# Performance work log

Hardware: AMD Instinct MI355X
Metric: run time of the kernel (lower is better)

## Reference

```python
import jax, jax.numpy as jnp
import numpy as np

B, IN_DIM, HID, OUT_DIM = 32768, 784, 256, 1000
L, CURV = 3, 1e-3
LOG2_H = 8  # log2(HID)
EPS_BN = 1e-5

def _layer_param_sizes():
    return [(HID // (2 * (1 << (l % LOG2_H)))) * 2 for l in range(L)]

def setup_inputs():
    key = jax.random.key(0)
    ks = jax.random.split(key, 4)
    total = sum(_layer_param_sizes())  # 448
    return {
        "x": jax.random.normal(ks[0], (B, IN_DIM), jnp.float32),
        "fc1_w": jax.random.normal(ks[1], (HID, IN_DIM), jnp.float32) / np.sqrt(IN_DIM).astype(np.float32),
        "fc1_b": jnp.zeros((HID,), jnp.float32),
        "bn1_gamma": jnp.ones((HID,), jnp.float32),
        "bn1_beta": jnp.zeros((HID,), jnp.float32),
        "bf_params": jax.random.normal(ks[2], (total,), jnp.float32) * 0.01,
        "bn2_gamma": jnp.ones((HID,), jnp.float32),
        "bn2_beta": jnp.zeros((HID,), jnp.float32),
        "fc2_w": jax.random.normal(ks[3], (OUT_DIM, HID), jnp.float32) / np.sqrt(HID).astype(np.float32),
        "fc2_b": jnp.zeros((OUT_DIM,), jnp.float32),
    }

def _batchnorm(h, gamma, beta):
    # training-mode BatchNorm1d: batch mean / biased variance
    mu = jnp.mean(h, axis=0)
    var = jnp.mean(jnp.square(h - mu), axis=0)
    return gamma * (h - mu) * jax.lax.rsqrt(var + EPS_BN) + beta

def _log_map0(x, c):
    # Poincare ball log map at origin: artanh(sqrt(c)|x|) * x / (sqrt(c)|x|)
    sn = jnp.sqrt(c) * jnp.linalg.norm(x, axis=-1, keepdims=True)
    sn = jnp.clip(sn, 1e-7, 1.0 - 1e-6)
    return (jnp.arctanh(sn) / sn) * x

def _exp_map0(u, c):
    sn = jnp.maximum(jnp.sqrt(c) * jnp.linalg.norm(u, axis=-1, keepdims=True), 1e-7)
    return (jnp.tanh(sn) / sn) * u

def _hyper_butterfly(h, params, c):
    u = _log_map0(h, c)
    off = 0
    for l in range(L):
        bs = 1 << (l % LOG2_H)      # half-block size at stage l
        nb = HID // (2 * bs)        # number of 2x2-rotation blocks
        p = params[off:off + 2 * nb]
        a = p[:nb][None, :, None]   # [1, nb, 1]
        b = p[nb:][None, :, None]
        v = u.reshape(-1, nb, 2, bs)
        x1, x2 = v[:, :, 0], v[:, :, 1]
        y1 = a * x1 + b * x2
        y2 = -b * x1 + a * x2
        u = jnp.stack([y1, y2], axis=2).reshape(-1, HID)
        off += 2 * nb
    return _exp_map0(u, c)

def reference(x, fc1_w, fc1_b, bn1_gamma, bn1_beta, bf_params, bn2_gamma, bn2_beta, fc2_w, fc2_b):
    h = x @ fc1_w.T + fc1_b
    h = jax.nn.relu(_batchnorm(h, bn1_gamma, bn1_beta))
    ht = _hyper_butterfly(h, bf_params, CURV)
    ht = jax.nn.relu(_batchnorm(ht, bn2_gamma, bn2_beta))
    return ht @ fc2_w.T + fc2_b
```

## Files before the change

### kernel.cpp

```cpp
#include <hip/hip_runtime.h>
#include <math.h>

#define NBATCH 32768
#define IND    784
#define KPAD1  832
#define HIDD   256
#define OUTD   1000
#define OUTDP  1024

typedef _Float16 half8  __attribute__((ext_vector_type(8)));
typedef _Float16 half4v __attribute__((ext_vector_type(4)));
typedef float    floatx4 __attribute__((ext_vector_type(4)));

#define GAS __attribute__((address_space(1)))
#define LAS __attribute__((address_space(3)))

#define WAITVM(N) asm volatile("s_waitcnt vmcnt(" #N ")" ::: "memory")
#define WAITVM_BAR(N)                                                      \
    asm volatile("s_waitcnt vmcnt(" #N ") lgkmcnt(0)" ::: "memory");       \
    __builtin_amdgcn_s_barrier();                                          \
    __builtin_amdgcn_sched_barrier(0)

__device__ __forceinline__ void gld16(const void* g, void* l) {
    __builtin_amdgcn_global_load_lds((const GAS void*)g, (LAS void*)l, 16, 0, 0);
}

__device__ __forceinline__ float wave_allreduce_sum(float v) {
    #pragma unroll
    for (int off = 32; off >= 1; off >>= 1) v += __shfl_xor(v, off);
    return v;
}

__device__ __forceinline__ float fast_atanh(float s) {
    return 0.5f * __logf((1.0f + s) * __frcp_rn(1.0f - s));
}
__device__ __forceinline__ float fast_tanh(float x) {
    const float e = __expf(-2.0f * x);
    return (1.0f - e) * __frcp_rn(1.0f + e);
}

__global__ __launch_bounds__(256)
void prep_kernel(const float* __restrict__ w1, _Float16* __restrict__ w1h,
                 const float* __restrict__ w2, _Float16* __restrict__ w2h,
                 float* __restrict__ stat)
{
    const int tid = threadIdx.x;
    if (blockIdx.x == 0) {
        for (int j = tid; j < 1024 + 16; j += 256) stat[j] = 0.0f;
    }
    const int NW1 = HIDD * (KPAD1 / 8);
    const int NW2 = OUTDP * (HIDD / 8);
    for (int i = blockIdx.x * 256 + tid; i < NW1 + NW2; i += (int)gridDim.x * 256) {
        half8 o;
        if (i < NW1) {
            const int r = i / (KPAD1 / 8), c8 = (i % (KPAD1 / 8)) * 8;
            if (c8 + 8 <= IND) {
                const float* s = &w1[(size_t)r * IND + c8];
                float4 v0 = *(const float4*)s, v1 = *(const float4*)(s + 4);
                o[0]=(_Float16)v0.x; o[1]=(_Float16)v0.y; o[2]=(_Float16)v0.z; o[3]=(_Float16)v0.w;
                o[4]=(_Float16)v1.x; o[5]=(_Float16)v1.y; o[6]=(_Float16)v1.z; o[7]=(_Float16)v1.w;
            } else {
                #pragma unroll
                for (int j = 0; j < 8; ++j) o[j] = (_Float16)0.0f;
            }
            *(half8*)&w1h[(size_t)r * KPAD1 + c8] = o;
        } else {
            const int k = i - NW1;
            const int r = k >> 5, c8 = (k & 31) * 8;
            if (r < OUTD) {
                const float* s = &w2[(size_t)r * HIDD + c8];
                float4 v0 = *(const float4*)s, v1 = *(const float4*)(s + 4);
                o[0]=(_Float16)v0.x; o[1]=(_Float16)v0.y; o[2]=(_Float16)v0.z; o[3]=(_Float16)v0.w;
                o[4]=(_Float16)v1.x; o[5]=(_Float16)v1.y; o[6]=(_Float16)v1.z; o[7]=(_Float16)v1.w;
            } else {
                #pragma unroll
                for (int j = 0; j < 8; ++j) o[j] = (_Float16)0.0f;
            }
            *(half8*)&w2h[(size_t)r * HIDD + c8] = o;
        }
    }
}

__global__ __launch_bounds__(256, 2)
void gemm1_kernel(const float* __restrict__ x, const _Float16* __restrict__ w1h,
                  const float* __restrict__ b1, const float* __restrict__ zbuf,
                  _Float16* __restrict__ h16, float* __restrict__ sum1, float* __restrict__ ssq1)
{
    __shared__ __align__(16) _Float16 ldsA[2][8192];
    __shared__ __align__(16) _Float16 ldsB[2][8192];
    __shared__ float redS[2][128], redQ[2][128];

    const int tid  = threadIdx.x;
    const int bid0 = blockIdx.x;
    const int vbid = (bid0 & 7) * 64 + (bid0 >> 3);
    const int bm = vbid >> 1, bn = vbid & 1;
    const int m0 = bm * 128, n0 = bn * 128;
    const int lane = tid & 63, wv = tid >> 6;
    const int wr = wv >> 1, wc = wv & 1;
    const int l15 = lane & 15, lg = lane >> 4;
    const int e3 = l15 & 3;
    const int nt = KPAD1 / 64;

    const int r0g = tid >> 2, r1g = 64 + (tid >> 2), kq = tid & 3;
    const int wpos0 = r0g * 32 + ((kq ^ (r0g & 3)) * 8);
    const int wpos1 = r1g * 32 + ((kq ^ (r1g & 3)) * 8);
    const float* Ab0 = x + (size_t)(m0 + r0g) * IND + kq * 8;
    const float* Ab1 = x + (size_t)(m0 + r1g) * IND + kq * 8;

    const int brow = lane >> 2, bgp = (lane & 3) ^ (brow & 3);
    const _Float16* Bb = w1h + (size_t)(n0 + brow) * KPAD1 + bgp * 8;

    floatx4 acc[4][4];
    #pragma unroll
    for (int i = 0; i < 4; ++i)
        #pragma unroll
        for (int j = 0; j < 4; ++j) acc[i][j] = (floatx4){0.f, 0.f, 0.f, 0.f};

    floatx4 rgaE[8], rgaO[8];

    auto A_ISSUE = [&](floatx4 (&rg)[8], int t) {
        #pragma unroll
        for (int ks = 0; ks < 2; ++ks) {
            const int off = t * 64 + ks * 32;
            const bool v = (off + kq * 8) < IND;
            const float* p0 = v ? (Ab0 + off) : zbuf;
            const float* p1 = v ? (Ab1 + off) : zbuf;
            rg[ks*4+0] = *(const floatx4*)p0;
            rg[ks*4+1] = *(const floatx4*)(p0 + 4);
            rg[ks*4+2] = *(const floatx4*)p1;
            rg[ks*4+3] = *(const floatx4*)(p1 + 4);
        }
    };
    auto A_WRITE = [&](floatx4 (&rg)[8], int wb) {
        #pragma unroll
        for (int ks = 0; ks < 2; ++ks) {
            half8 h0, h1;
            #pragma unroll
            for (int j = 0; j < 4; ++j) {
                h0[j] = (_Float16)rg[ks*4+0][j]; h0[4+j] = (_Float16)rg[ks*4+1][j];
                h1[j] = (_Float16)rg[ks*4+2][j]; h1[4+j] = (_Float16)rg[ks*4+3][j];
            }
            *(half8*)&ldsA[wb][ks * 4096 + wpos0] = h0;
            *(half8*)&ldsA[wb][ks * 4096 + wpos1] = h1;
        }
    };
    auto B_ISSUE = [&](int bb, int t) {
        const bool tok = t < nt;
        #pragma unroll
        for (int ks = 0; ks < 2; ++ks)
            #pragma unroll
            for (int c = 0; c < 2; ++c) {
                const int ch = wv + c * 4;
                const void* s = tok ? (const void*)(Bb + (size_t)ch * 16 * KPAD1 + t * 64 + ks * 32)
                                    : (const void*)zbuf;
                gld16(s, &ldsB[bb][ks * 4096 + ch * 512]);
            }
    };
    auto COMPUTE = [&](int abuf, int brd) {
        #pragma unroll
        for (int ks = 0; ks < 2; ++ks) {
            half8 af[4], bfr[4];
            #pragma unroll
            for (int i = 0; i < 4; ++i)
                af[i] = *(const half8*)&ldsA[abuf][ks*4096 + (wr*64 + i*16 + l15)*32 + ((lg ^ e3)*8)];
            #pragma unroll
            for (int j = 0; j < 4; ++j)
                bfr[j] = *(const half8*)&ldsB[brd][ks*4096 + (wc*4 + j)*512 + l15*32 + ((lg ^ e3)*8)];
            #pragma unroll
            for (int i = 0; i < 4; ++i)
                #pragma unroll
                for (int j = 0; j < 4; ++j)
                    acc[i][j] = __builtin_amdgcn_mfma_f32_16x16x32_f16(bfr[j], af[i], acc[i][j], 0, 0, 0);
        }
    };

    A_ISSUE(rgaE, 0);
    B_ISSUE(0, 0);
    WAITVM(4);
    A_WRITE(rgaE, 0);
    A_ISSUE(rgaO, 1);
    WAITVM_BAR(8);

    for (int p = 0; p < 6; ++p) {
        const int t = p * 2;
        B_ISSUE(1, t + 1);
        A_ISSUE(rgaE, t + 2);
        COMPUTE(0, 0);
        __builtin_amdgcn_sched_barrier(0);
        WAITVM(8);
        A_WRITE(rgaO, 1);
        WAITVM_BAR(8);
        B_ISSUE(0, t + 2);
        A_ISSUE(rgaO, t + 3);
        COMPUTE(1, 1);
        __builtin_amdgcn_sched_barrier(0);
        WAITVM(8);
        A_WRITE(rgaE, 0);
        WAITVM_BAR(8);
    }
    COMPUTE(0, 0);
    WAITVM(0);

    float sJ[4][4], qJ[4][4];
    #pragma unroll
    for (int j = 0; j < 4; ++j)
        #pragma unroll
        for (int r = 0; r < 4; ++r) { sJ[j][r] = 0.f; qJ[j][r] = 0.f; }
    #pragma unroll
    for (int i = 0; i < 4; ++i) {
        const int m = m0 + wr * 64 + i * 16 + l15;
        #pragma unroll
        for (int j = 0; j < 4; ++j) {
            const int nb = n0 + wc * 64 + j * 16 + lg * 4;
            float4 bt = *reinterpret_cast<const float4*>(&b1[nb]);
            float v[4] = {acc[i][j][0] + bt.x, acc[i][j][1] + bt.y,
                          acc[i][j][2] + bt.z, acc[i][j][3] + bt.w};
            half4v hv;
            hv[0] = (_Float16)v[0]; hv[1] = (_Float16)v[1];
            hv[2] = (_Float16)v[2]; hv[3] = (_Float16)v[3];
            *reinterpret_cast<half4v*>(&h16[(size_t)m * HIDD + nb]) = hv;
            #pragma unroll
            for (int r = 0; r < 4; ++r) { sJ[j][r] += v[r]; qJ[j][r] += v[r] * v[r]; }
        }
    }
    #pragma unroll
    for (int j = 0; j < 4; ++j)
        #pragma unroll
        for (int r = 0; r < 4; ++r) {
            float s = sJ[j][r], q = qJ[j][r];
            s += __shfl_xor(s, 1); s += __shfl_xor(s, 2);
            s += __shfl_xor(s, 4); s += __shfl_xor(s, 8);
            q += __shfl_xor(q, 1); q += __shfl_xor(q, 2);
            q += __shfl_xor(q, 4); q += __shfl_xor(q, 8);
            if (l15 == 0) {
                redS[wr][wc * 64 + j * 16 + lg * 4 + r] = s;
                redQ[wr][wc * 64 + j * 16 + lg * 4 + r] = q;
            }
        }
    __syncthreads();
    if (tid < 128) {
        atomicAdd(&sum1[n0 + tid], redS[0][tid] + redS[1][tid]);
        atomicAdd(&ssq1[n0 + tid], redQ[0][tid] + redQ[1][tid]);
    }
}

__global__ __launch_bounds__(256)
void mid_kernel(const _Float16* __restrict__ h16, const float* __restrict__ bfp,
                const float* __restrict__ sum1, const float* __restrict__ ssq1,
                const float* __restrict__ g1, const float* __restrict__ be1,
                _Float16* __restrict__ ht16, float* __restrict__ sum2, float* __restrict__ ssq2)
{
    __shared__ float s1sh[256], t1sh[256];
    __shared__ float bsum[4][256], bssq[4][256];
    const int tid  = threadIdx.x;
    {
        const float inv = 1.0f / (float)NBATCH;
        const float mu  = sum1[tid] * inv;
        const float var = fmaxf(ssq1[tid] * inv - mu * mu, 0.0f);
        const float rs  = 1.0f / sqrtf(var + 1e-5f);
        const float sj  = g1[tid] * rs;
        s1sh[tid] = sj;
        t1sh[tid] = fmaf(-mu, sj, be1[tid]);
    }
    __syncthreads();

    const int w    = tid >> 6;
    const int lane = tid & 63;
    const int row0 = blockIdx.x * 32 + w * 8;
    const int c0   = lane * 4;

    const float4 s1v = *reinterpret_cast<const float4*>(&s1sh[c0]);
    const float4 t1v = *reinterpret_cast<const float4*>(&t1sh[c0]);
    const float a0 = bfp[2 * lane],       a1 = bfp[2 * lane + 1];
    const float b0 = bfp[128 + 2 * lane], b1 = bfp[128 + 2 * lane + 1];
    const float a2 = bfp[256 + lane],     b2 = bfp[320 + lane];
    const float a3 = bfp[384 + (lane >> 1)], b3 = bfp[416 + (lane >> 1)];
    const float sgn = (lane & 1) ? -1.0f : 1.0f;
    const float sc  = sqrtf(1e-3f);

    float ps0 = 0, ps1 = 0, ps2 = 0, ps3 = 0;
    float q0 = 0, q1 = 0, q2 = 0, q3 = 0;

    for (int r = 0; r < 8; ++r) {
        const int row = row0 + r;
        half4v hv4 = *reinterpret_cast<const half4v*>(&h16[(size_t)row * HIDD + c0]);
        float x0 = fmaxf(fmaf((float)hv4[0], s1v.x, t1v.x), 0.0f);
        float x1 = fmaxf(fmaf((float)hv4[1], s1v.y, t1v.y), 0.0f);
        float x2 = fmaxf(fmaf((float)hv4[2], s1v.z, t1v.z), 0.0f);
        float x3 = fmaxf(fmaf((float)hv4[3], s1v.w, t1v.w), 0.0f);
        float n2 = x0 * x0 + x1 * x1 + x2 * x2 + x3 * x3;
        n2 = wave_allreduce_sum(n2);
        float sn = sc * sqrtf(n2);
        sn = fminf(fmaxf(sn, 1e-7f), 1.0f - 1e-6f);
        const float ls = fast_atanh(sn) * __frcp_rn(sn);
        x0 *= ls; x1 *= ls; x2 *= ls; x3 *= ls;
        const float y0 = fmaf(a0, x0,  b0 * x1);
        const float y1 = fmaf(a0, x1, -b0 * x0);
        const float y2 = fmaf(a1, x2,  b1 * x3);
        const float y3 = fmaf(a1, x3, -b1 * x2);
        const float z0 = fmaf(a2, y0,  b2 * y2);
        const float z1 = fmaf(a2, y1,  b2 * y3);
        const float z2 = fmaf(a2, y2, -b2 * y0);
        const float z3 = fmaf(a2, y3, -b2 * y1);
        const float p0 = __shfl_xor(z0, 1);
        const float p1 = __shfl_xor(z1, 1);
        const float p2 = __shfl_xor(z2, 1);
        const float p3 = __shfl_xor(z3, 1);
        const float w0 = fmaf(a3, z0, sgn * (b3 * p0));
        const float w1 = fmaf(a3, z1, sgn * (b3 * p1));
        const float w2 = fmaf(a3, z2, sgn * (b3 * p2));
        const float w3 = fmaf(a3, z3, sgn * (b3 * p3));
        float m2 = w0 * w0 + w1 * w1 + w2 * w2 + w3 * w3;
        m2 = wave_allreduce_sum(m2);
        const float sn2 = fmaxf(sc * sqrtf(m2), 1e-7f);
        const float es = fast_tanh(sn2) * __frcp_rn(sn2);
        const float o0 = es * w0, o1 = es * w1, o2 = es * w2, o3 = es * w3;
        half4v hv;
        hv[0] = (_Float16)(o0 * 65536.0f); hv[1] = (_Float16)(o1 * 65536.0f);
        hv[2] = (_Float16)(o2 * 65536.0f); hv[3] = (_Float16)(o3 * 65536.0f);
        *reinterpret_cast<half4v*>(&ht16[(size_t)row * HIDD + c0]) = hv;
        ps0 += o0; ps1 += o1; ps2 += o2; ps3 += o3;
        q0 += o0 * o0; q1 += o1 * o1; q2 += o2 * o2; q3 += o3 * o3;
    }

    bsum[w][c0 + 0] = ps0; bsum[w][c0 + 1] = ps1; bsum[w][c0 + 2] = ps2; bsum[w][c0 + 3] = ps3;
    bssq[w][c0 + 0] = q0;  bssq[w][c0 + 1] = q1;  bssq[w][c0 + 2] = q2;  bssq[w][c0 + 3] = q3;
    __syncthreads();
    if (tid < 256) {
        const float s = bsum[0][tid] + bsum[1][tid] + bsum[2][tid] + bsum[3][tid];
        const float q = bssq[0][tid] + bssq[1][tid] + bssq[2][tid] + bssq[3][tid];
        atomicAdd(&sum2[tid], s);
        atomicAdd(&ssq2[tid], q);
    }
}

__global__ __launch_bounds__(256, 3)
void gemm2_kernel(const _Float16* __restrict__ ht16, const _Float16* __restrict__ w2h,
                  const float* __restrict__ b2,
                  const float* __restrict__ sum2, const float* __restrict__ ssq2,
                  const float* __restrict__ g2, const float* __restrict__ be2,
                  const float* __restrict__ zbuf, float* __restrict__ out)
{
    __shared__ __align__(16) _Float16 ldsA[3][4096];
    __shared__ __align__(16) _Float16 ldsB[3][4096];
    __shared__ float sf[256], tf[256];

    const int tid = threadIdx.x;
    {
        const float inv = 1.0f / (float)NBATCH;
        const float mu  = sum2[tid] * inv;
        const float var = fmaxf(ssq2[tid] * inv - mu * mu, 0.0f);
        const float rs  = 1.0f / sqrtf(var + 1e-5f);
        const float sj  = g2[tid] * rs;
        sf[tid] = sj * (1024.0f / 65536.0f);
        tf[tid] = fmaf(-mu, sj, be2[tid]) * 1024.0f;
    }

    const int bid0 = blockIdx.x;
    const int vbid = (bid0 & 7) * 256 + (bid0 >> 3);
    const int bm = vbid >> 3, bn = vbid & 7;
    const int m0 = bm * 128, n0 = bn * 128;
    const int lane = tid & 63, wv = tid >> 6;
    const int wr = wv >> 1, wc = wv & 1;
    const int l15 = lane & 15, lg = lane >> 4;
    const int e3 = l15 & 3;
    const int nt = HIDD / 32;

    const int srow = lane >> 2, sgp = (lane & 3) ^ (srow & 3);
    const _Float16* Ab = ht16 + (size_t)(m0 + srow) * HIDD + sgp * 8;
    const _Float16* Bb = w2h  + (size_t)(n0 + srow) * HIDD + sgp * 8;

    floatx4 acc[4][4];
    #pragma unroll
    for (int i = 0; i < 4; ++i)
        #pragma unroll
        for (int j = 0; j < 4; ++j) acc[i][j] = (floatx4){0.f, 0.f, 0.f, 0.f};

    auto STAGE = [&](int buf, int t) {
        const int t32 = t * 32;
        const bool tok = t < nt;
        #pragma unroll
        for (int c = 0; c < 2; ++c) {
            const int ch = wv + c * 4;
            const void* sa = tok ? (const void*)(Ab + (size_t)ch * 16 * HIDD + t32)
                                 : (const void*)zbuf;
            const void* sb = tok ? (const void*)(Bb + (size_t)ch * 16 * HIDD + t32)
                                 : (const void*)zbuf;
            gld16(sa, &ldsA[buf][ch * 512]);
            gld16(sb, &ldsB[buf][ch * 512]);
        }
    };

    STAGE(0, 0);
    STAGE(1, 1);
    WAITVM_BAR(4);

    int buf = 0;
    for (int t = 0; t < nt; ++t) {
        int nbuf = buf + 2; if (nbuf >= 3) nbuf -= 3;
        STAGE(nbuf, t + 2);
        const int kb = t * 32 + lg * 8;
        float4 s0 = *(const float4*)&sf[kb], s1 = *(const float4*)&sf[kb + 4];
        float4 t0 = *(const float4*)&tf[kb], t1 = *(const float4*)&tf[kb + 4];
        half8 af[4], bfr[4];
        #pragma unroll
        for (int i = 0; i < 4; ++i) {
            half8 v = *(const half8*)&ldsA[buf][(wr * 4 + i) * 512 + l15 * 32 + ((lg ^ e3) * 8)];
            half8 hv;
            hv[0] = (_Float16)fmaxf(fmaf((float)v[0], s0.x, t0.x), 0.0f);
            hv[1] = (_Float16)fmaxf(fmaf((float)v[1], s0.y, t0.y), 0.0f);
            hv[2] = (_Float16)fmaxf(fmaf((float)v[2], s0.z, t0.z), 0.0f);
            hv[3] = (_Float16)fmaxf(fmaf((float)v[3], s0.w, t0.w), 0.0f);
            hv[4] = (_Float16)fmaxf(fmaf((float)v[4], s1.x, t1.x), 0.0f);
            hv[5] = (_Float16)fmaxf(fmaf((float)v[5], s1.y, t1.y), 0.0f);
            hv[6] = (_Float16)fmaxf(fmaf((float)v[6], s1.z, t1.z), 0.0f);
            hv[7] = (_Float16)fmaxf(fmaf((float)v[7], s1.w, t1.w), 0.0f);
            af[i] = hv;
        }
        #pragma unroll
        for (int j = 0; j < 4; ++j)
            bfr[j] = *(const half8*)&ldsB[buf][(wc * 4 + j) * 512 + l15 * 32 + ((lg ^ e3) * 8)];
        #pragma unroll
        for (int i = 0; i < 4; ++i)
            #pragma unroll
            for (int j = 0; j < 4; ++j)
                acc[i][j] = __builtin_amdgcn_mfma_f32_16x16x32_f16(bfr[j], af[i], acc[i][j], 0, 0, 0);
        WAITVM_BAR(4);
        buf = (buf + 1 == 3) ? 0 : buf + 1;
    }
    WAITVM(0);

    const float invScale = 1.0f / 1024.0f;
    #pragma unroll
    for (int i = 0; i < 4; ++i) {
        const int m = m0 + wr * 64 + i * 16 + l15;
        #pragma unroll
        for (int j = 0; j < 4; ++j) {
            const int nb = n0 + wc * 64 + j * 16 + lg * 4;
            float bj[4];
            if (nb + 4 <= OUTD) {
                float4 bt = *reinterpret_cast<const float4*>(&b2[nb]);
                bj[0] = bt.x; bj[1] = bt.y; bj[2] = bt.z; bj[3] = bt.w;
            } else {
                #pragma unroll
                for (int r = 0; r < 4; ++r) bj[r] = (nb + r < OUTD) ? b2[nb + r] : 0.0f;
            }
            float v[4];
            #pragma unroll
            for (int r = 0; r < 4; ++r) v[r] = fmaf(acc[i][j][r], invScale, bj[r]);
            if (nb + 4 <= OUTD) {
                *reinterpret_cast<float4*>(&out[(size_t)m * OUTD + nb]) =
                    make_float4(v[0], v[1], v[2], v[3]);
            } else {
                #pragma unroll
                for (int r = 0; r < 4; ++r)
                    if (nb + r < OUTD) out[(size_t)m * OUTD + nb + r] = v[r];
            }
        }
    }
}

extern "C" void kernel_launch(void* const* d_in, const int* in_sizes, int n_in,
                              void* d_out, int out_size, void* d_ws, size_t ws_size,
                              hipStream_t stream)
{
    const float* x   = (const float*)d_in[0];
    const float* w1  = (const float*)d_in[1];
    const float* b1  = (const float*)d_in[2];
    const float* g1  = (const float*)d_in[3];
    const float* be1 = (const float*)d_in[4];
    const float* bfp = (const float*)d_in[5];
    const float* g2  = (const float*)d_in[6];
    const float* be2 = (const float*)d_in[7];
    const float* w2  = (const float*)d_in[8];
    const float* b2  = (const float*)d_in[9];

    float* out = (float*)d_out;
    char*  wsb = (char*)d_ws;

    _Float16* ht16 = (_Float16*)(wsb);
    _Float16* w1h  = (_Float16*)(wsb + 16777216);
    _Float16* w2h  = (_Float16*)(wsb + 17203200);
    float*    stat = (float*)  (wsb + 17727488);
    float* sum1 = stat;
    float* ssq1 = stat + 256;
    float* sum2 = stat + 512;
    float* ssq2 = stat + 768;
    float* zbuf = stat + 1024;

    _Float16* h16 = (_Float16*)out;

    prep_kernel<<<232, 256, 0, stream>>>(w1, w1h, w2, w2h, stat);
    gemm1_kernel<<<512, 256, 0, stream>>>(x, w1h, b1, zbuf, h16, sum1, ssq1);
    mid_kernel<<<1024, 256, 0, stream>>>(h16, bfp, sum1, ssq1, g1, be1, ht16, sum2, ssq2);
    gemm2_kernel<<<2048, 256, 0, stream>>>(ht16, w2h, b2, sum2, ssq2, g2, be2, zbuf, out);
}
```

Measured before the change: 126.4 us.

## Use full-width 128x256 tiles in gemm1 with 512 threads and K-step 32

The first GEMM now has each block compute a 128-row by 256-column tile covering the whole hidden dimension, with 8 waves instead of 4. Each x tile is then read from global memory once instead of twice, and the K step is halved to 32 with a smaller K padding (800). This cuts redundant fp32 input traffic, which dominates this GEMM. In exchange, only 256 blocks are launched at one per CU, with more pipeline iterations and less latency hiding per CU.

```diff
diff --git a/kernel.cpp b/kernel.cpp
--- a/kernel.cpp
+++ b/kernel.cpp
@@ -3,7 +3,7 @@
 
 #define NBATCH 32768
 #define IND    784
-#define KPAD1  832
+#define KPAD1  800
 #define HIDD   256
 #define OUTD   1000
 #define OUTDP  1024
@@ -81,34 +81,31 @@
     }
 }
 
-__global__ __launch_bounds__(256, 2)
+__global__ __launch_bounds__(512, 1)
 void gemm1_kernel(const float* __restrict__ x, const _Float16* __restrict__ w1h,
                   const float* __restrict__ b1, const float* __restrict__ zbuf,
                   _Float16* __restrict__ h16, float* __restrict__ sum1, float* __restrict__ ssq1)
 {
-    __shared__ __align__(16) _Float16 ldsA[2][8192];
+    __shared__ __align__(16) _Float16 ldsA[2][4096];
     __shared__ __align__(16) _Float16 ldsB[2][8192];
-    __shared__ float redS[2][128], redQ[2][128];
+    __shared__ float redS[2][256], redQ[2][256];
 
     const int tid  = threadIdx.x;
     const int bid0 = blockIdx.x;
-    const int vbid = (bid0 & 7) * 64 + (bid0 >> 3);
-    const int bm = vbid >> 1, bn = vbid & 1;
-    const int m0 = bm * 128, n0 = bn * 128;
+    const int vbid = (bid0 & 7) * 32 + (bid0 >> 3);
+    const int m0 = vbid * 128;
     const int lane = tid & 63, wv = tid >> 6;
-    const int wr = wv >> 1, wc = wv & 1;
+    const int wr = wv >> 2, wc = wv & 3;
     const int l15 = lane & 15, lg = lane >> 4;
     const int e3 = l15 & 3;
-    const int nt = KPAD1 / 64;
-
-    const int r0g = tid >> 2, r1g = 64 + (tid >> 2), kq = tid & 3;
-    const int wpos0 = r0g * 32 + ((kq ^ (r0g & 3)) * 8);
-    const int wpos1 = r1g * 32 + ((kq ^ (r1g & 3)) * 8);
-    const float* Ab0 = x + (size_t)(m0 + r0g) * IND + kq * 8;
-    const float* Ab1 = x + (size_t)(m0 + r1g) * IND + kq * 8;
+    const int nt = KPAD1 / 32;
+
+    const int arow = tid >> 2, kq = tid & 3;
+    const int wpos = arow * 32 + ((kq ^ (arow & 3)) * 8);
+    const float* Ab = x + (size_t)(m0 + arow) * IND + kq * 8;
 
     const int brow = lane >> 2, bgp = (lane & 3) ^ (brow & 3);
-    const _Float16* Bb = w1h + (size_t)(n0 + brow) * KPAD1 + bgp * 8;
+    const _Float16* Bb = w1h + (size_t)brow * KPAD1 + bgp * 8;
 
     floatx4 acc[4][4];
     #pragma unroll
@@ -116,87 +113,69 @@
         #pragma unroll
         for (int j = 0; j < 4; ++j) acc[i][j] = (floatx4){0.f, 0.f, 0.f, 0.f};
 
-    floatx4 rgaE[8], rgaO[8];
-
-    auto A_ISSUE = [&](floatx4 (&rg)[8], int t) {
-        #pragma unroll
-        for (int ks = 0; ks < 2; ++ks) {
-            const int off = t * 64 + ks * 32;
-            const bool v = (off + kq * 8) < IND;
-            const float* p0 = v ? (Ab0 + off) : zbuf;
-            const float* p1 = v ? (Ab1 + off) : zbuf;
-            rg[ks*4+0] = *(const floatx4*)p0;
-            rg[ks*4+1] = *(const floatx4*)(p0 + 4);
-            rg[ks*4+2] = *(const floatx4*)p1;
-            rg[ks*4+3] = *(const floatx4*)(p1 + 4);
-        }
+    floatx4 rgaE[2], rgaO[2];
+
+    auto A_ISSUE = [&](floatx4 (&rg)[2], int t) {
+        const int off = t * 32;
+        const bool v = (off + kq * 8) < IND;
+        const float* p = v ? (Ab + off) : zbuf;
+        rg[0] = *(const floatx4*)p;
+        rg[1] = *(const floatx4*)(p + 4);
     };
-    auto A_WRITE = [&](floatx4 (&rg)[8], int wb) {
-        #pragma unroll
-        for (int ks = 0; ks < 2; ++ks) {
-            half8 h0, h1;
-            #pragma unroll
-            for (int j = 0; j < 4; ++j) {
-                h0[j] = (_Float16)rg[ks*4+0][j]; h0[4+j] = (_Float16)rg[ks*4+1][j];
-                h1[j] = (_Float16)rg[ks*4+2][j]; h1[4+j] = (_Float16)rg[ks*4+3][j];
-            }
-            *(half8*)&ldsA[wb][ks * 4096 + wpos0] = h0;
-            *(half8*)&ldsA[wb][ks * 4096 + wpos1] = h1;
-        }
+    auto A_WRITE = [&](floatx4 (&rg)[2], int wb) {
+        half8 hv;
+        #pragma unroll
+        for (int j = 0; j < 4; ++j) { hv[j] = (_Float16)rg[0][j]; hv[4+j] = (_Float16)rg[1][j]; }
+        *(half8*)&ldsA[wb][wpos] = hv;
     };
     auto B_ISSUE = [&](int bb, int t) {
         const bool tok = t < nt;
         #pragma unroll
-        for (int ks = 0; ks < 2; ++ks)
-            #pragma unroll
-            for (int c = 0; c < 2; ++c) {
-                const int ch = wv + c * 4;
-                const void* s = tok ? (const void*)(Bb + (size_t)ch * 16 * KPAD1 + t * 64 + ks * 32)
-                                    : (const void*)zbuf;
-                gld16(s, &ldsB[bb][ks * 4096 + ch * 512]);
-            }
+        for (int c = 0; c < 2; ++c) {
+            const int ch = wv + c * 8;
+            const void* s = tok ? (const void*)(Bb + (size_t)ch * 16 * KPAD1 + t * 32)
+                                : (const void*)zbuf;
+            gld16(s, &ldsB[bb][ch * 512]);
+        }
     };
     auto COMPUTE = [&](int abuf, int brd) {
-        #pragma unroll
-        for (int ks = 0; ks < 2; ++ks) {
-            half8 af[4], bfr[4];
-            #pragma unroll
-            for (int i = 0; i < 4; ++i)
-                af[i] = *(const half8*)&ldsA[abuf][ks*4096 + (wr*64 + i*16 + l15)*32 + ((lg ^ e3)*8)];
+        half8 af[4], bfr[4];
+        #pragma unroll
+        for (int i = 0; i < 4; ++i)
+            af[i] = *(const half8*)&ldsA[abuf][(wr * 64 + i * 16 + l15) * 32 + ((lg ^ e3) * 8)];
+        #pragma unroll
+        for (int j = 0; j < 4; ++j)
+            bfr[j] = *(const half8*)&ldsB[brd][(wc * 4 + j) * 512 + l15 * 32 + ((lg ^ e3) * 8)];
+        #pragma unroll
+        for (int i = 0; i < 4; ++i)
             #pragma unroll
             for (int j = 0; j < 4; ++j)
-                bfr[j] = *(const half8*)&ldsB[brd][ks*4096 + (wc*4 + j)*512 + l15*32 + ((lg ^ e3)*8)];
-            #pragma unroll
-            for (int i = 0; i < 4; ++i)
-                #pragma unroll
-                for (int j = 0; j < 4; ++j)
-                    acc[i][j] = __builtin_amdgcn_mfma_f32_16x16x32_f16(bfr[j], af[i], acc[i][j], 0, 0, 0);
-        }
+                acc[i][j] = __builtin_amdgcn_mfma_f32_16x16x32_f16(bfr[j], af[i], acc[i][j], 0, 0, 0);
     };
 
     A_ISSUE(rgaE, 0);
     B_ISSUE(0, 0);
-    WAITVM(4);
+    WAITVM(2);
     A_WRITE(rgaE, 0);
     A_ISSUE(rgaO, 1);
-    WAITVM_BAR(8);
-
-    for (int p = 0; p < 6; ++p) {
+    WAITVM_BAR(2);
+
+    for (int p = 0; p < 12; ++p) {
         const int t = p * 2;
         B_ISSUE(1, t + 1);
         A_ISSUE(rgaE, t + 2);
         COMPUTE(0, 0);
         __builtin_amdgcn_sched_barrier(0);
-        WAITVM(8);
+        WAITVM(2);
         A_WRITE(rgaO, 1);
-        WAITVM_BAR(8);
+        WAITVM_BAR(2);
         B_ISSUE(0, t + 2);
         A_ISSUE(rgaO, t + 3);
         COMPUTE(1, 1);
         __builtin_amdgcn_sched_barrier(0);
-        WAITVM(8);
+        WAITVM(2);
         A_WRITE(rgaE, 0);
-        WAITVM_BAR(8);
+        WAITVM_BAR(2);
     }
     COMPUTE(0, 0);
     WAITVM(0);
@@ -211,7 +190,7 @@
         const int m = m0 + wr * 64 + i * 16 + l15;
         #pragma unroll
         for (int j = 0; j < 4; ++j) {
-            const int nb = n0 + wc * 64 + j * 16 + lg * 4;
+            const int nb = wc * 64 + j * 16 + lg * 4;
             float4 bt = *reinterpret_cast<const float4*>(&b1[nb]);
             float v[4] = {acc[i][j][0] + bt.x, acc[i][j][1] + bt.y,
                           acc[i][j][2] + bt.z, acc[i][j][3] + bt.w};
@@ -238,9 +217,9 @@
             }
         }
     __syncthreads();
-    if (tid < 128) {
-        atomicAdd(&sum1[n0 + tid], redS[0][tid] + redS[1][tid]);
-        atomicAdd(&ssq1[n0 + tid], redQ[0][tid] + redQ[1][tid]);
+    if (tid < 256) {
+        atomicAdd(&sum1[tid], redS[0][tid] + redS[1][tid]);
+        atomicAdd(&ssq1[tid], redQ[0][tid] + redQ[1][tid]);
     }
 }
 
@@ -480,8 +459,8 @@
 
     _Float16* ht16 = (_Float16*)(wsb);
     _Float16* w1h  = (_Float16*)(wsb + 16777216);
-    _Float16* w2h  = (_Float16*)(wsb + 17203200);
-    float*    stat = (float*)  (wsb + 17727488);
+    _Float16* w2h  = (_Float16*)(wsb + 17186816);
+    float*    stat = (float*)  (wsb + 17711104);
     float* sum1 = stat;
     float* ssq1 = stat + 256;
     float* sum2 = stat + 512;
@@ -491,7 +470,7 @@
     _Float16* h16 = (_Float16*)out;
 
     prep_kernel<<<232, 256, 0, stream>>>(w1, w1h, w2, w2h, stat);
-    gemm1_kernel<<<512, 256, 0, stream>>>(x, w1h, b1, zbuf, h16, sum1, ssq1);
+    gemm1_kernel<<<256, 512, 0, stream>>>(x, w1h, b1, zbuf, h16, sum1, ssq1);
     mid_kernel<<<1024, 256, 0, stream>>>(h16, bfp, sum1, ssq1, g1, be1, ht16, sum2, ssq2);
     gemm2_kernel<<<2048, 256, 0, stream>>>(ht16, w2h, b2, sum2, ssq2, g2, be2, zbuf, out);
 }
```

New measurement: 132.5 us. 4.8% more time.
